# Kernel tuning notes

Hardware: AMD Instinct MI355X
Metric: run time of the kernel (lower is better)

The kernel has to match this reference:

```python
import jax, jax.numpy as jnp
import numpy as np

H = 16
D_MODEL = 1024
D_K = D_MODEL // H  # 64


def setup_inputs() -> dict:
    key = jax.random.key(0)
    ks = jax.random.split(key, 8)
    B, S = 8, 1024
    q = jax.random.normal(ks[0], (B, S, D_MODEL), dtype=jnp.float32)
    k = jax.random.normal(ks[1], (B, S, D_MODEL), dtype=jnp.float32)
    v = jax.random.normal(ks[2], (B, S, D_MODEL), dtype=jnp.float32)
    # xavier_normal for [h, d_model, d_k]: std = sqrt(2 / (d_model + d_k)) (fan over last two dims)
    std_p = float(np.sqrt(2.0 / (D_MODEL + D_K)))
    W_q = jax.random.normal(ks[3], (H, D_MODEL, D_K), dtype=jnp.float32) * std_p
    W_k = jax.random.normal(ks[4], (H, D_MODEL, D_K), dtype=jnp.float32) * std_p
    W_v = jax.random.normal(ks[5], (H, D_MODEL, D_K), dtype=jnp.float32) * std_p
    std_o = float(np.sqrt(2.0 / (H * D_K + D_MODEL)))
    W_o = jax.random.normal(ks[6], (D_MODEL, H * D_K), dtype=jnp.float32) * std_o  # torch Linear weight [out, in]
    b_o = jax.random.normal(ks[7], (D_MODEL,), dtype=jnp.float32) * 0.01
    return {"q": q, "k": k, "v": v, "W_q": W_q, "W_k": W_k, "W_v": W_v, "W_o": W_o, "b_o": b_o}


def reference(q, k, v, W_q, W_k, W_v, W_o, b_o):
    B, S, _ = q.shape
    # per-head projections: [h, b, s, d_k]
    qh = jnp.einsum('bsd,hdk->hbsk', q, W_q)
    kh = jnp.einsum('bsd,hdk->hbsk', k, W_k)
    vh = jnp.einsum('bsd,hdk->hbsk', v, W_v)
    scale = 1.0 / jnp.sqrt(jnp.asarray(D_K, dtype=q.dtype))
    scores = jnp.einsum('hbsk,hbtk->hbst', qh, kh) * scale  # [h,b,s,s]
    attn = jax.nn.softmax(scores, axis=-1)
    c = jnp.einsum('hbst,hbtk->hbsk', attn, vh)  # [h,b,s,d_k]
    # torch code splits the stacked (h*b) batch and concats on feature dim:
    # head index becomes the OUTER factor of the feature dim -> [b,s,h*d_k]
    c = jnp.transpose(c, (1, 2, 0, 3)).reshape(B, S, H * D_K)
    out = c @ W_o.T + b_o
    return out
```

## Files before the change

### kernel.cpp

```cpp
#include <hip/hip_runtime.h>
#include <hip/hip_bf16.h>

typedef __bf16 bf16_t;
typedef __attribute__((ext_vector_type(8))) __bf16 bf16x8;
typedef __attribute__((ext_vector_type(4))) float f32x4;

#define MFMA(a, b, c) __builtin_amdgcn_mfma_f32_16x16x32_bf16(a, b, c, 0, 0, 0)

__global__ void fill_sentinel(float* out, int n, float val) {
  int i = blockIdx.x * blockDim.x + threadIdx.x;
  if (i < n) out[i] = val;
}

__global__ void transpose_w(const float* __restrict__ Wq, const float* __restrict__ Wk,
                            const float* __restrict__ Wv, bf16_t* __restrict__ Wt) {
  int gid = blockIdx.x * blockDim.x + threadIdx.x;
  int e = gid * 8;
  int m = e >> 20;
  int rem = e & 1048575;
  int n = rem >> 10;
  int d0 = rem & 1023;
  const float* W = (m == 0) ? Wq : (m == 1) ? Wk : Wv;
  int h = n >> 6, kk = n & 63;
  union { bf16_t h8[8]; uint4 u; } tmp;
#pragma unroll
  for (int j = 0; j < 8; ++j)
    tmp.h8[j] = (bf16_t)W[((size_t)(h * 1024 + d0 + j)) * 64 + kk];
  *(uint4*)(Wt + e) = tmp.u;
}

__device__ inline bf16x8 ld8(const bf16_t* p) { return *(const bf16x8*)p; }
__device__ inline bf16x8 ld8(const float* p) {
  f32x4 a = *(const f32x4*)p;
  f32x4 b = *(const f32x4*)(p + 4);
  bf16x8 r;
  r[0] = (bf16_t)a[0]; r[1] = (bf16_t)a[1]; r[2] = (bf16_t)a[2]; r[3] = (bf16_t)a[3];
  r[4] = (bf16_t)b[0]; r[5] = (bf16_t)b[1]; r[6] = (bf16_t)b[2]; r[7] = (bf16_t)b[3];
  return r;
}

template <int MODE, typename TA>
__global__ void gemm_bt(const TA* __restrict__ A, const void* __restrict__ Bt_,
                        const float* __restrict__ bias, void* __restrict__ out_,
                        int M, int N, int K) {
  constexpr int PAD = 40;
  __shared__ bf16_t sA[128 * PAD];
  __shared__ bf16_t sB[128 * PAD];
  const int t = threadIdx.x;
  const int w = t >> 6, l = t & 63;
  const int lq = l >> 4, ll = l & 15;
  const int m0 = blockIdx.x * 128, n0 = blockIdx.y * 128;
  const int wr = (w >> 1) * 64, wc = (w & 1) * 64;
  f32x4 acc[4][4] = {};
  for (int k0 = 0; k0 < K; k0 += 32) {
    __syncthreads();
#pragma unroll
    for (int r = 0; r < 2; ++r) {
      int e = (r * 256 + t) * 8;
      int row = e >> 5, col = e & 31;
      *(bf16x8*)(sA + row * PAD + col) = ld8(A + (size_t)(m0 + row) * K + k0 + col);
      if (MODE == 2)
        *(bf16x8*)(sB + row * PAD + col) =
            ld8((const float*)Bt_ + (size_t)(n0 + row) * K + k0 + col);
      else
        *(bf16x8*)(sB + row * PAD + col) =
            ld8((const bf16_t*)Bt_ + (size_t)(n0 + row) * K + k0 + col);
    }
    __syncthreads();
    bf16x8 af[4], bfr[4];
#pragma unroll
    for (int i = 0; i < 4; ++i) {
      af[i]  = *(const bf16x8*)(sA + (wr + i * 16 + ll) * PAD + lq * 8);
      bfr[i] = *(const bf16x8*)(sB + (wc + i * 16 + ll) * PAD + lq * 8);
    }
#pragma unroll
    for (int mi = 0; mi < 4; ++mi)
#pragma unroll
      for (int ni = 0; ni < 4; ++ni)
        acc[mi][ni] = MFMA(af[mi], bfr[ni], acc[mi][ni]);
  }
#pragma unroll
  for (int mi = 0; mi < 4; ++mi)
#pragma unroll
    for (int ni = 0; ni < 4; ++ni)
#pragma unroll
      for (int r = 0; r < 4; ++r) {
        int row = m0 + wr + mi * 16 + lq * 4 + r;
        int col = n0 + wc + ni * 16 + ll;
        float v = acc[mi][ni][r];
        if (MODE == 2) {
          ((float*)out_)[(size_t)row * N + col] = v + bias[col];
        } else {
          int h = col >> 6, kk = col & 63, b = row >> 10, s = row & 1023;
          size_t idx;
          if (MODE == 0)
            idx = ((size_t)((h * 8 + b) * 1024 + s)) * 64 + kk;
          else
            idx = ((size_t)((h * 8 + b) * 64 + kk)) * 1024 + s;
          ((bf16_t*)out_)[idx] = (bf16_t)v;
        }
      }
}

__global__ void attn_kernel(const bf16_t* __restrict__ qh, const bf16_t* __restrict__ kh,
                            const bf16_t* __restrict__ vt, bf16_t* __restrict__ c) {
  constexpr int QP = 72, KP = 72, VP = 136, PP = 136;
  __shared__ bf16_t sQ[64 * QP];
  __shared__ bf16_t sK[128 * KP];
  __shared__ bf16_t sV[64 * VP];
  __shared__ bf16_t sP[4][16 * PP];
  const int t = threadIdx.x;
  const int w = t >> 6, l = t & 63;
  const int lq = l >> 4, ll = l & 15;
  const int q0 = blockIdx.x * 64;
  const int hb = blockIdx.y;
  const int h = hb >> 3, b = hb & 7;
  const size_t base = (size_t)hb * 65536;
  const bf16_t* Q = qh + base + (size_t)q0 * 64;
  const bf16_t* K = kh + base;
  const bf16_t* V = vt + base;
#pragma unroll
  for (int r = 0; r < 2; ++r) {
    int e = (r * 256 + t) * 8;
    int row = e >> 6, col = e & 63;
    *(uint4*)(sQ + row * QP + col) = *(const uint4*)(Q + e);
  }
  float mrow[4], lrow[4];
  f32x4 o[4] = {};
#pragma unroll
  for (int r = 0; r < 4; ++r) { mrow[r] = -1e30f; lrow[r] = 0.f; }

  for (int kt = 0; kt < 1024; kt += 128) {
    __syncthreads();
#pragma unroll
    for (int r = 0; r < 4; ++r) {
      int e = (r * 256 + t) * 8;
      int row = e >> 6, col = e & 63;
      *(uint4*)(sK + row * KP + col) = *(const uint4*)(K + (size_t)kt * 64 + e);
      int rowv = e >> 7, colv = e & 127;
      *(uint4*)(sV + rowv * VP + colv) =
          *(const uint4*)(V + (size_t)rowv * 1024 + kt + colv);
    }
    __syncthreads();
    f32x4 sacc[8] = {};
    bf16x8 aq[2];
#pragma unroll
    for (int ks = 0; ks < 2; ++ks)
      aq[ks] = *(const bf16x8*)(sQ + (w * 16 + ll) * QP + ks * 32 + lq * 8);
#pragma unroll
    for (int ni = 0; ni < 8; ++ni)
#pragma unroll
      for (int ks = 0; ks < 2; ++ks) {
        bf16x8 bk = *(const bf16x8*)(sK + (ni * 16 + ll) * KP + ks * 32 + lq * 8);
        sacc[ni] = MFMA(aq[ks], bk, sacc[ni]);
      }
    float rmax[4] = {-1e30f, -1e30f, -1e30f, -1e30f};
#pragma unroll
    for (int ni = 0; ni < 8; ++ni)
#pragma unroll
      for (int r = 0; r < 4; ++r) {
        sacc[ni][r] *= 0.125f;
        rmax[r] = fmaxf(rmax[r], sacc[ni][r]);
      }
#pragma unroll
    for (int off = 1; off < 16; off <<= 1)
#pragma unroll
      for (int r = 0; r < 4; ++r)
        rmax[r] = fmaxf(rmax[r], __shfl_xor(rmax[r], off));
    float alpha[4];
#pragma unroll
    for (int r = 0; r < 4; ++r) {
      float mnew = fmaxf(mrow[r], rmax[r]);
      alpha[r] = __expf(mrow[r] - mnew);
      mrow[r] = mnew;
    }
    float rs[4] = {0.f, 0.f, 0.f, 0.f};
#pragma unroll
    for (int ni = 0; ni < 8; ++ni)
#pragma unroll
      for (int r = 0; r < 4; ++r) {
        float p = __expf(sacc[ni][r] - mrow[r]);
        sacc[ni][r] = p;
        rs[r] += p;
      }
#pragma unroll
    for (int off = 1; off < 16; off <<= 1)
#pragma unroll
      for (int r = 0; r < 4; ++r)
        rs[r] += __shfl_xor(rs[r], off);
#pragma unroll
    for (int r = 0; r < 4; ++r)
      lrow[r] = lrow[r] * alpha[r] + rs[r];
#pragma unroll
    for (int ni = 0; ni < 4; ++ni)
#pragma unroll
      for (int r = 0; r < 4; ++r)
        o[ni][r] *= alpha[r];
    bf16_t* Pw = sP[w];
#pragma unroll
    for (int ni = 0; ni < 8; ++ni)
#pragma unroll
      for (int r = 0; r < 4; ++r)
        Pw[(lq * 4 + r) * PP + ni * 16 + ll] = (bf16_t)sacc[ni][r];
    asm volatile("s_waitcnt lgkmcnt(0)" ::: "memory");
#pragma unroll
    for (int ks = 0; ks < 4; ++ks) {
      bf16x8 ap = *(const bf16x8*)(Pw + ll * PP + ks * 32 + lq * 8);
#pragma unroll
      for (int ni = 0; ni < 4; ++ni) {
        bf16x8 bv = *(const bf16x8*)(sV + (ni * 16 + ll) * VP + ks * 32 + lq * 8);
        o[ni] = MFMA(ap, bv, o[ni]);
      }
    }
  }
#pragma unroll
  for (int ni = 0; ni < 4; ++ni)
#pragma unroll
    for (int r = 0; r < 4; ++r) {
      int s = q0 + w * 16 + lq * 4 + r;
      int dk = ni * 16 + ll;
      float val = o[ni][r] / lrow[r];
      c[((size_t)(b * 1024 + s)) * 1024 + h * 64 + dk] = (bf16_t)val;
    }
}

extern "C" void kernel_launch(void* const* d_in, const int* in_sizes, int n_in,
                              void* d_out, int out_size, void* d_ws, size_t ws_size,
                              hipStream_t stream) {
  float* out = (float*)d_out;
  int nblk_out = (out_size + 255) / 256;
  if (n_in != 8) {
    fill_sentinel<<<nblk_out, 256, 0, stream>>>(out, out_size, 600.0f + 10.0f * n_in);
    return;
  }
  const int expect[8] = {8388608, 8388608, 8388608, 1048576,
                         1048576, 1048576, 1048576, 1024};
  for (int i = 0; i < 8; ++i)
    if (in_sizes[i] != expect[i]) {
      fill_sentinel<<<nblk_out, 256, 0, stream>>>(out, out_size, 500.0f + 10.0f * i);
      return;
    }

  bf16_t* ws   = (bf16_t*)d_ws;
  bf16_t* qhb  = ws;
  bf16_t* khb  = ws + 8388608;
  bf16_t* vtb  = ws + 16777216;
  bf16_t* Wt   = ws + 25165824;
  bf16_t* cbuf = ws + 25165824;
  if (ws_size < 67108864ull) {
    fill_sentinel<<<nblk_out, 256, 0, stream>>>(out, out_size, 400.0f);
    return;
  }

  const float* q  = (const float*)d_in[0];
  const float* k  = (const float*)d_in[1];
  const float* v  = (const float*)d_in[2];
  const float* Wq = (const float*)d_in[3];
  const float* Wk = (const float*)d_in[4];
  const float* Wv = (const float*)d_in[5];
  const float* Wo = (const float*)d_in[6];
  const float* bo = (const float*)d_in[7];

  transpose_w<<<1536, 256, 0, stream>>>(Wq, Wk, Wv, Wt);
  dim3 gg(64, 8);
  gemm_bt<0, float><<<gg, 256, 0, stream>>>(q, Wt,           nullptr, qhb, 8192, 1024, 1024);
  gemm_bt<0, float><<<gg, 256, 0, stream>>>(k, Wt + 1048576, nullptr, khb, 8192, 1024, 1024);
  gemm_bt<1, float><<<gg, 256, 0, stream>>>(v, Wt + 2097152, nullptr, vtb, 8192, 1024, 1024);
  attn_kernel<<<dim3(16, 128), 256, 0, stream>>>(qhb, khb, vtb, cbuf);
  gemm_bt<2, bf16_t><<<gg, 256, 0, stream>>>(cbuf, Wo, bo, out, 8192, 1024, 1024);
}
```

Baseline: 473.7 us.

## Pre-convert GEMM inputs to bf16 and use direct global-to-LDS loads

Adds separate fp32-to-bf16 conversion kernels for q, k, v and W_o, staged in the output buffer and workspace, so every GEMM operand is bf16. The GEMM mainloop then fills shared memory with the global_load_lds builtin, 16 bytes per lane, in place of register-staged loads with in-loop conversion. The unpadded LDS layout may add bank conflicts on fragment reads. The extra conversion passes add memory traffic, and reusing the output and workspace buffers as scratch relies on careful lifetime ordering.

```diff
diff --git a/kernel.cpp b/kernel.cpp
--- a/kernel.cpp
+++ b/kernel.cpp
@@ -6,6 +6,12 @@
 typedef __attribute__((ext_vector_type(4))) float f32x4;
 
 #define MFMA(a, b, c) __builtin_amdgcn_mfma_f32_16x16x32_bf16(a, b, c, 0, 0, 0)
+
+__device__ inline void gload_lds16(const bf16_t* g, bf16_t* l) {
+  __builtin_amdgcn_global_load_lds(
+      (const __attribute__((address_space(1))) void*)g,
+      (__attribute__((address_space(3))) void*)l, 16, 0, 0);
+}
 
 __global__ void fill_sentinel(float* out, int n, float val) {
   int i = blockIdx.x * blockDim.x + threadIdx.x;
@@ -29,49 +35,45 @@
   *(uint4*)(Wt + e) = tmp.u;
 }
 
-__device__ inline bf16x8 ld8(const bf16_t* p) { return *(const bf16x8*)p; }
-__device__ inline bf16x8 ld8(const float* p) {
-  f32x4 a = *(const f32x4*)p;
-  f32x4 b = *(const f32x4*)(p + 4);
+__global__ void cvt_bf16(const float* __restrict__ in, bf16_t* __restrict__ out) {
+  size_t i = (size_t)(blockIdx.x * blockDim.x + threadIdx.x) * 8;
+  f32x4 a = *(const f32x4*)(in + i);
+  f32x4 b = *(const f32x4*)(in + i + 4);
   bf16x8 r;
   r[0] = (bf16_t)a[0]; r[1] = (bf16_t)a[1]; r[2] = (bf16_t)a[2]; r[3] = (bf16_t)a[3];
   r[4] = (bf16_t)b[0]; r[5] = (bf16_t)b[1]; r[6] = (bf16_t)b[2]; r[7] = (bf16_t)b[3];
-  return r;
-}
-
-template <int MODE, typename TA>
-__global__ void gemm_bt(const TA* __restrict__ A, const void* __restrict__ Bt_,
+  *(bf16x8*)(out + i) = r;
+}
+
+template <int MODE>
+__global__ void gemm_bt(const bf16_t* __restrict__ A, const bf16_t* __restrict__ Bt,
                         const float* __restrict__ bias, void* __restrict__ out_,
                         int M, int N, int K) {
-  constexpr int PAD = 40;
-  __shared__ bf16_t sA[128 * PAD];
-  __shared__ bf16_t sB[128 * PAD];
+  __shared__ bf16_t sA[128 * 32];
+  __shared__ bf16_t sB[128 * 32];
   const int t = threadIdx.x;
   const int w = t >> 6, l = t & 63;
   const int lq = l >> 4, ll = l & 15;
   const int m0 = blockIdx.x * 128, n0 = blockIdx.y * 128;
   const int wr = (w >> 1) * 64, wc = (w & 1) * 64;
+  const int srow = l >> 2;
+  const int scol = (l & 3) * 8;
   f32x4 acc[4][4] = {};
   for (int k0 = 0; k0 < K; k0 += 32) {
     __syncthreads();
 #pragma unroll
-    for (int r = 0; r < 2; ++r) {
-      int e = (r * 256 + t) * 8;
-      int row = e >> 5, col = e & 31;
-      *(bf16x8*)(sA + row * PAD + col) = ld8(A + (size_t)(m0 + row) * K + k0 + col);
-      if (MODE == 2)
-        *(bf16x8*)(sB + row * PAD + col) =
-            ld8((const float*)Bt_ + (size_t)(n0 + row) * K + k0 + col);
-      else
-        *(bf16x8*)(sB + row * PAD + col) =
-            ld8((const bf16_t*)Bt_ + (size_t)(n0 + row) * K + k0 + col);
+    for (int c = 0; c < 2; ++c) {
+      int ch = w * 2 + c;
+      int row = ch * 16 + srow;
+      gload_lds16(A  + (size_t)(m0 + row) * K + k0 + scol, sA + ch * 512);
+      gload_lds16(Bt + (size_t)(n0 + row) * K + k0 + scol, sB + ch * 512);
     }
     __syncthreads();
     bf16x8 af[4], bfr[4];
 #pragma unroll
     for (int i = 0; i < 4; ++i) {
-      af[i]  = *(const bf16x8*)(sA + (wr + i * 16 + ll) * PAD + lq * 8);
-      bfr[i] = *(const bf16x8*)(sB + (wc + i * 16 + ll) * PAD + lq * 8);
+      af[i]  = *(const bf16x8*)(sA + (wr + i * 16 + ll) * 32 + lq * 8);
+      bfr[i] = *(const bf16x8*)(sB + (wc + i * 16 + ll) * 32 + lq * 8);
     }
 #pragma unroll
     for (int mi = 0; mi < 4; ++mi)
@@ -247,6 +249,7 @@
   bf16_t* vtb  = ws + 16777216;
   bf16_t* Wt   = ws + 25165824;
   bf16_t* cbuf = ws + 25165824;
+  bf16_t* Wob  = ws;
   if (ws_size < 67108864ull) {
     fill_sentinel<<<nblk_out, 256, 0, stream>>>(out, out_size, 400.0f);
     return;
@@ -261,11 +264,19 @@
   const float* Wo = (const float*)d_in[6];
   const float* bo = (const float*)d_in[7];
 
+  bf16_t* qb = (bf16_t*)d_out;
+  bf16_t* kb = (bf16_t*)d_out + 8388608;
+  bf16_t* vb = (bf16_t*)d_out;
+
   transpose_w<<<1536, 256, 0, stream>>>(Wq, Wk, Wv, Wt);
+  cvt_bf16<<<4096, 256, 0, stream>>>(q, qb);
+  cvt_bf16<<<4096, 256, 0, stream>>>(k, kb);
   dim3 gg(64, 8);
-  gemm_bt<0, float><<<gg, 256, 0, stream>>>(q, Wt,           nullptr, qhb, 8192, 1024, 1024);
-  gemm_bt<0, float><<<gg, 256, 0, stream>>>(k, Wt + 1048576, nullptr, khb, 8192, 1024, 1024);
-  gemm_bt<1, float><<<gg, 256, 0, stream>>>(v, Wt + 2097152, nullptr, vtb, 8192, 1024, 1024);
+  gemm_bt<0><<<gg, 256, 0, stream>>>(qb, Wt,           nullptr, qhb, 8192, 1024, 1024);
+  gemm_bt<0><<<gg, 256, 0, stream>>>(kb, Wt + 1048576, nullptr, khb, 8192, 1024, 1024);
+  cvt_bf16<<<4096, 256, 0, stream>>>(v, vb);
+  gemm_bt<1><<<gg, 256, 0, stream>>>(vb, Wt + 2097152, nullptr, vtb, 8192, 1024, 1024);
   attn_kernel<<<dim3(16, 128), 256, 0, stream>>>(qhb, khb, vtb, cbuf);
-  gemm_bt<2, bf16_t><<<gg, 256, 0, stream>>>(cbuf, Wo, bo, out, 8192, 1024, 1024);
-}
+  cvt_bf16<<<512, 256, 0, stream>>>(Wo, Wob);
+  gemm_bt<2><<<gg, 256, 0, stream>>>(cbuf, Wob, bo, out, 8192, 1024, 1024);
+}
```

Measured after the change: 438.2 us. 1.08x faster.
